# Optimization experiments

Measured on AMD Instinct MI355X. Metric: run time of the kernel, lower is better.

## Reference

```python
import jax, jax.numpy as jnp
import numpy as np

D_MODEL = 1024
N_HEADS = 16
D_K = D_MODEL // N_HEADS
ROPE_BASE = 10000.0


def rope_cos_sin(seq_len, d_k, base=ROPE_BASE, dtype=jnp.float32):
    inv_freq = 1.0 / (base ** (jnp.arange(0, d_k, 2, dtype=dtype) / d_k))  # [d_k/2]
    pos = jnp.arange(seq_len, dtype=dtype)
    freqs = jnp.outer(pos, inv_freq)  # [T, d_k/2]
    return jnp.cos(freqs), jnp.sin(freqs)


def apply_rope(x, cos, sin):
    # x: [B, H, T, d_k]; cos/sin: [T, d_k/2]
    x1 = x[..., 0::2]
    x2 = x[..., 1::2]
    c = cos[None, None]
    s = sin[None, None]
    r1 = x1 * c - x2 * s
    r2 = x1 * s + x2 * c
    # interleave back: stack on new last axis then flatten
    return jnp.stack([r1, r2], axis=-1).reshape(x.shape)


def setup_inputs() -> dict:
    key = jax.random.key(0)
    ks = jax.random.split(key, 7)
    B, T = 2, 2048
    q = jax.random.normal(ks[0], (B, T, D_MODEL), dtype=jnp.float32)
    k = jax.random.normal(ks[1], (B, T, D_MODEL), dtype=jnp.float32)
    v = jax.random.normal(ks[2], (B, T, D_MODEL), dtype=jnp.float32)
    scale = 1.0 / np.sqrt(D_MODEL)
    W_q = jax.random.normal(ks[3], (D_MODEL, D_MODEL), dtype=jnp.float32) * scale
    W_k = jax.random.normal(ks[4], (D_MODEL, D_MODEL), dtype=jnp.float32) * scale
    W_v = jax.random.normal(ks[5], (D_MODEL, D_MODEL), dtype=jnp.float32) * scale
    W_o = jax.random.normal(ks[6], (D_MODEL, D_MODEL), dtype=jnp.float32) * scale
    return {"q": q, "k": k, "v": v, "W_q": W_q, "W_k": W_k, "W_v": W_v, "W_o": W_o}


def reference(q, k, v, W_q, W_k, W_v, W_o):
    B, T_q, _ = q.shape
    T_k = k.shape[1]
    # Linear (torch stores weight as [out, in]; y = x @ W.T)
    Q = (q @ W_q.T).reshape(B, T_q, N_HEADS, D_K).transpose(0, 2, 1, 3)
    K = (k @ W_k.T).reshape(B, T_k, N_HEADS, D_K).transpose(0, 2, 1, 3)
    V = (v @ W_v.T).reshape(B, T_k, N_HEADS, D_K).transpose(0, 2, 1, 3)
    cos_q, sin_q = rope_cos_sin(T_q, D_K)
    cos_k, sin_k = rope_cos_sin(T_k, D_K)
    Q = apply_rope(Q, cos_q, sin_q)
    K = apply_rope(K, cos_k, sin_k)
    scale = jnp.sqrt(jnp.asarray(D_K, dtype=Q.dtype))
    scores = jnp.einsum('bhqd,bhkd->bhqk', Q, K) / scale  # [B,H,Tq,Tk]
    attn = jax.nn.softmax(scores, axis=-1)
    out = jnp.einsum('bhqk,bhkd->bhqd', attn, V)
    out = out.transpose(0, 2, 1, 3).reshape(B, T_q, D_MODEL)
    return out @ W_o.T
```

## Files before the change

kernel.cpp:

```cpp
#include <hip/hip_runtime.h>
#include <math.h>

#define D_MODEL 1024
#define NHEADS  16
#define DK      64
#define TT      2048
#define BB      2
#define MM      (BB * TT)
#define SEG     ((size_t)4194304)
#define WSEG    ((size_t)1048576)

typedef __attribute__((ext_vector_type(8))) short bf16x8;
typedef __attribute__((ext_vector_type(4))) float f32x4;
typedef __attribute__((ext_vector_type(4))) uint  u32x4;

__device__ __forceinline__ ushort f2bf(float f) {
    union { float f; uint u; } v; v.f = f;
    return (ushort)((v.u + 0x7FFFu + ((v.u >> 16) & 1u)) >> 16);
}
__device__ __forceinline__ float bf2f(ushort h) {
    union { uint u; float f; } v; v.u = (uint)h << 16;
    return v.f;
}
__device__ __forceinline__ uint packbf(float lo, float hi) {
    return (uint)f2bf(lo) | ((uint)f2bf(hi) << 16);
}
__device__ __forceinline__ void gld16(ushort* lds, const ushort* g) {
    __builtin_amdgcn_global_load_lds(
        (const __attribute__((address_space(1))) void*)g,
        (__attribute__((address_space(3))) void*)lds, 16, 0, 0);
}
__device__ __forceinline__ void split2(float x, ushort& h, ushort& l) {
    h = f2bf(x);
    l = f2bf(x - bf2f(h));
}

__global__ __launch_bounds__(256) void cast_w_kernel(
    const float* __restrict__ wq, const float* __restrict__ wk,
    const float* __restrict__ wv, const float* __restrict__ wo,
    ushort* __restrict__ WH, ushort* __restrict__ WL)
{
    const int a = blockIdx.y;
    const float* src = (a == 0) ? wq : (a == 1) ? wk : (a == 2) ? wv : wo;
    ushort* hi = WH + (size_t)a * WSEG;
    ushort* lo = WL + (size_t)a * WSEG;
    const size_t i = ((size_t)blockIdx.x * 256 + threadIdx.x) * 8;
#pragma unroll
    for (int c = 0; c < 2; ++c) {
        float4 f = *(const float4*)&src[i + 4 * c];
        ushort4 uh, ul;
        split2(f.x, uh.x, ul.x); split2(f.y, uh.y, ul.y);
        split2(f.z, uh.z, ul.z); split2(f.w, uh.w, ul.w);
        *(ushort4*)&hi[i + 4 * c] = uh;
        *(ushort4*)&lo[i + 4 * c] = ul;
    }
}

__global__ __launch_bounds__(256) void cast_a_kernel(
    const float* __restrict__ src, ushort* __restrict__ hi, ushort* __restrict__ lo)
{
    const size_t i = ((size_t)blockIdx.x * 256 + threadIdx.x) * 8;
#pragma unroll
    for (int c = 0; c < 2; ++c) {
        float4 f = *(const float4*)&src[i + 4 * c];
        ushort4 uh, ul;
        split2(f.x, uh.x, ul.x); split2(f.y, uh.y, ul.y);
        split2(f.z, uh.z, ul.z); split2(f.w, uh.w, ul.w);
        *(ushort4*)&hi[i + 4 * c] = uh;
        *(ushort4*)&lo[i + 4 * c] = ul;
    }
}

template<int MODE>
__global__ __launch_bounds__(256) void gemm_kernel(
    const ushort* __restrict__ Ah, const ushort* __restrict__ Al,
    const ushort* __restrict__ Wh, const ushort* __restrict__ Wl,
    ushort* __restrict__ dst_bf, float* __restrict__ dst_f32)
{
    __shared__ ushort AsH[128 * 64];
    __shared__ ushort AsL[128 * 64];
    __shared__ ushort BsH[128 * 64];
    __shared__ ushort BsL[128 * 64];

    const int tid = threadIdx.x, lane = tid & 63, w = tid >> 6;
    const int g = lane >> 4, l15 = lane & 15;
    const int m0 = blockIdx.y << 7, n0 = blockIdx.x << 7;
    const int mw = (w >> 1) << 6, nw = (w & 1) << 6;

    int sOff[4], sBase[4];
#pragma unroll
    for (int i = 0; i < 4; ++i) {
        const int s = w * 256 + i * 64 + lane;
        const int r = s >> 3;
        sOff[i]  = r * 1024 + (((s & 7) ^ (r & 7)) << 3);
        sBase[i] = (w * 256 + i * 64) << 3;
    }

    const int p0 = (g ^ (l15 & 7)) << 3;
    const int p1 = ((4 + g) ^ (l15 & 7)) << 3;

    f32x4 acc[4][4] = {};

    for (int k0 = 0; k0 < 1024; k0 += 64) {
        const ushort* pA = (size_t)m0 * 1024 + k0 + Ah;
        const ushort* pa = (size_t)m0 * 1024 + k0 + Al;
        const ushort* pW = (size_t)n0 * 1024 + k0 + Wh;
        const ushort* pw = (size_t)n0 * 1024 + k0 + Wl;
#pragma unroll
        for (int i = 0; i < 4; ++i) {
            gld16(&AsH[sBase[i]], pA + sOff[i]);
            gld16(&AsL[sBase[i]], pa + sOff[i]);
            gld16(&BsH[sBase[i]], pW + sOff[i]);
            gld16(&BsL[sBase[i]], pw + sOff[i]);
        }
        __syncthreads();

#pragma unroll
        for (int ks = 0; ks < 2; ++ks) {
            const int pk = ks ? p1 : p0;
            bf16x8 ah[4], al[4];
#pragma unroll
            for (int j = 0; j < 4; ++j) {
                ah[j] = *(const bf16x8*)&AsH[(mw + 16 * j + l15) * 64 + pk];
                al[j] = *(const bf16x8*)&AsL[(mw + 16 * j + l15) * 64 + pk];
            }
#pragma unroll
            for (int i = 0; i < 4; ++i) {
                bf16x8 wh = *(const bf16x8*)&BsH[(nw + 16 * i + l15) * 64 + pk];
                bf16x8 wl = *(const bf16x8*)&BsL[(nw + 16 * i + l15) * 64 + pk];
#pragma unroll
                for (int j = 0; j < 4; ++j) {
                    if (MODE == 1) {
                        acc[j][i] = __builtin_amdgcn_mfma_f32_16x16x32_bf16(ah[j], wh, acc[j][i], 0, 0, 0);
                        acc[j][i] = __builtin_amdgcn_mfma_f32_16x16x32_bf16(ah[j], wl, acc[j][i], 0, 0, 0);
                        acc[j][i] = __builtin_amdgcn_mfma_f32_16x16x32_bf16(al[j], wh, acc[j][i], 0, 0, 0);
                    } else {
                        acc[i][j] = __builtin_amdgcn_mfma_f32_16x16x32_bf16(wh, ah[j], acc[i][j], 0, 0, 0);
                        acc[i][j] = __builtin_amdgcn_mfma_f32_16x16x32_bf16(wl, ah[j], acc[i][j], 0, 0, 0);
                        acc[i][j] = __builtin_amdgcn_mfma_f32_16x16x32_bf16(wh, al[j], acc[i][j], 0, 0, 0);
                    }
                }
            }
        }
        __syncthreads();
    }

    if (MODE == 0) {
        const float lb_over_dk = 9.210340371976184f / 64.0f;
#pragma unroll
        for (int ni = 0; ni < 4; ++ni) {
            const int nG = n0 + nw + 16 * ni + 4 * g;
            const int h  = nG >> 6;
            const int d0 = nG & 63;
            const float inv0 = __expf(-(float)(d0)     * lb_over_dk);
            const float inv1 = __expf(-(float)(d0 + 2) * lb_over_dk);
#pragma unroll
            for (int mj = 0; mj < 4; ++mj) {
                const int tG = m0 + mw + 16 * mj + l15;
                const int t  = tG & (TT - 1);
                const int b  = tG >> 11;
                const f32x4 x = acc[ni][mj];
                float c0, s0, c1, s1;
                __sincosf((float)t * inv0, &s0, &c0);
                __sincosf((float)t * inv1, &s1, &c1);
                ushort4 o;
                o.x = f2bf(x[0] * c0 - x[1] * s0);
                o.y = f2bf(x[0] * s0 + x[1] * c0);
                o.z = f2bf(x[2] * c1 - x[3] * s1);
                o.w = f2bf(x[2] * s1 + x[3] * c1);
                *(ushort4*)&dst_bf[(((size_t)b * NHEADS + h) * TT + t) * DK + d0] = o;
            }
        }
    } else if (MODE == 1) {
#pragma unroll
        for (int mi = 0; mi < 4; ++mi) {
            const int tG = m0 + mw + 16 * mi + 4 * g;
            const int t  = tG & (TT - 1);
            const int b  = tG >> 11;
#pragma unroll
            for (int nj = 0; nj < 4; ++nj) {
                const int nG = n0 + nw + 16 * nj + l15;
                const int h  = nG >> 6;
                const int d  = nG & 63;
                const f32x4 x = acc[mi][nj];
                ushort4 o = {f2bf(x[0]), f2bf(x[1]), f2bf(x[2]), f2bf(x[3])};
                *(ushort4*)&dst_bf[(((size_t)b * NHEADS + h) * DK + d) * TT + t] = o;
            }
        }
    } else {
#pragma unroll
        for (int ni = 0; ni < 4; ++ni) {
            const int nG = n0 + nw + 16 * ni + 4 * g;
#pragma unroll
            for (int mj = 0; mj < 4; ++mj) {
                const int m = m0 + mw + 16 * mj + l15;
                const f32x4 x = acc[ni][mj];
                *(float4*)&dst_f32[(size_t)m * D_MODEL + nG] = make_float4(x[0], x[1], x[2], x[3]);
            }
        }
    }
}

__global__ __launch_bounds__(256) void attn_kernel(
    const ushort* __restrict__ Qw, const ushort* __restrict__ Kw,
    const ushort* __restrict__ Vtw, ushort* __restrict__ ctxH, ushort* __restrict__ ctxL)
{
    __shared__ ushort Ks[64 * 64];
    __shared__ ushort Vs[64 * 64];

    const int tid  = threadIdx.x;
    const int lane = tid & 63;
    const int w    = tid >> 6;
    const int qi   = lane & 15;
    const int g    = lane >> 4;
    const int bh   = blockIdx.y;
    const int q0   = blockIdx.x << 6;

    const ushort* Qp = Qw  + (size_t)bh * TT * DK;
    const ushort* Kp = Kw  + (size_t)bh * TT * DK;
    const ushort* Vp = Vtw + (size_t)bh * DK * TT;

    const int qrow = q0 + w * 16 + qi;
    bf16x8 qf0 = *(const bf16x8*)&Qp[(size_t)qrow * DK + 8 * g];
    bf16x8 qf1 = *(const bf16x8*)&Qp[(size_t)qrow * DK + 32 + 8 * g];

    float m_i = -INFINITY, l_i = 0.0f;
    f32x4 o[4] = {};

    const int c0row = tid >> 3, c0col = tid & 7;
    const int c1row = (tid + 256) >> 3, c1col = tid & 7;
    const int sw0 = (c0col ^ (c0row & 7)) << 3;
    const int sw1 = (c1col ^ (c1row & 7)) << 3;

    for (int kt = 0; kt < TT; kt += 64) {
        *(float4*)&Ks[c0row * 64 + sw0] = *(const float4*)&Kp[(size_t)(kt + c0row) * DK + c0col * 8];
        *(float4*)&Ks[c1row * 64 + sw1] = *(const float4*)&Kp[(size_t)(kt + c1row) * DK + c1col * 8];
        *(float4*)&Vs[c0row * 64 + sw0] = *(const float4*)&Vp[(size_t)c0row * TT + kt + c0col * 8];
        *(float4*)&Vs[c1row * 64 + sw1] = *(const float4*)&Vp[(size_t)c1row * TT + kt + c1col * 8];
        __syncthreads();

        float sv[4][4];
#pragma unroll
        for (int c = 0; c < 4; ++c) {
            f32x4 acc = {};
            const int row = c * 16 + qi;
#pragma unroll
            for (int s = 0; s < 2; ++s) {
                const int col16 = (4 * s + g) ^ (row & 7);
                bf16x8 kf = *(const bf16x8*)&Ks[row * 64 + col16 * 8];
                acc = __builtin_amdgcn_mfma_f32_16x16x32_bf16(kf, (s == 0) ? qf0 : qf1, acc, 0, 0, 0);
            }
#pragma unroll
            for (int r = 0; r < 4; ++r) sv[c][r] = acc[r] * 0.125f;
        }

        float mt = fmaxf(fmaxf(fmaxf(sv[0][0], sv[0][1]), fmaxf(sv[0][2], sv[0][3])),
                         fmaxf(fmaxf(sv[1][0], sv[1][1]), fmaxf(sv[1][2], sv[1][3])));
        mt = fmaxf(mt, fmaxf(fmaxf(fmaxf(sv[2][0], sv[2][1]), fmaxf(sv[2][2], sv[2][3])),
                             fmaxf(fmaxf(sv[3][0], sv[3][1]), fmaxf(sv[3][2], sv[3][3]))));
        mt = fmaxf(mt, __shfl_xor(mt, 16));
        mt = fmaxf(mt, __shfl_xor(mt, 32));
        const float mnew  = fmaxf(m_i, mt);
        const float alpha = __expf(m_i - mnew);
        m_i = mnew;

        float rs = 0.0f;
        uint pp[4][2];
#pragma unroll
        for (int c = 0; c < 4; ++c) {
            float p0 = __expf(sv[c][0] - mnew);
            float p1 = __expf(sv[c][1] - mnew);
            float p2 = __expf(sv[c][2] - mnew);
            float p3 = __expf(sv[c][3] - mnew);
            rs += (p0 + p1) + (p2 + p3);
            pp[c][0] = packbf(p0, p1);
            pp[c][1] = packbf(p2, p3);
        }
        rs += __shfl_xor(rs, 16);
        rs += __shfl_xor(rs, 32);
        l_i = l_i * alpha + rs;
#pragma unroll
        for (int dt = 0; dt < 4; ++dt)
#pragma unroll
            for (int r = 0; r < 4; ++r) o[dt][r] *= alpha;

#pragma unroll
        for (int s = 0; s < 2; ++s) {
            uint bu[4];
#pragma unroll
            for (int v = 0; v < 4; ++v) {
                const int srcl = ((2 * (g & 1) + (v >> 1)) << 4) + qi;
                const uint a = __shfl(pp[2 * s][v & 1], srcl);
                const uint b = __shfl(pp[2 * s + 1][v & 1], srcl);
                bu[v] = (g >> 1) ? b : a;
            }
            u32x4 bu4 = {bu[0], bu[1], bu[2], bu[3]};
            bf16x8 pf = __builtin_bit_cast(bf16x8, bu4);
#pragma unroll
            for (int dt = 0; dt < 4; ++dt) {
                const int row = dt * 16 + qi;
                const int col16 = (4 * s + g) ^ (row & 7);
                bf16x8 vf = *(const bf16x8*)&Vs[row * 64 + col16 * 8];
                o[dt] = __builtin_amdgcn_mfma_f32_16x16x32_bf16(vf, pf, o[dt], 0, 0, 0);
            }
        }
        __syncthreads();
    }

    const float inv = 1.0f / l_i;
    const int b = bh >> 4, h = bh & 15;
    const size_t base = ((size_t)b * TT + qrow) * D_MODEL + h * DK;
#pragma unroll
    for (int dt = 0; dt < 4; ++dt) {
        ushort4 oh, ol;
#pragma unroll
        for (int r = 0; r < 4; ++r) {
            float val = o[dt][r] * inv;
            ushort hh, ll; split2(val, hh, ll);
            ((ushort*)&oh)[r] = hh;
            ((ushort*)&ol)[r] = ll;
        }
        *(ushort4*)&ctxH[base + dt * 16 + 4 * g] = oh;
        *(ushort4*)&ctxL[base + dt * 16 + 4 * g] = ol;
    }
}

extern "C" void kernel_launch(void* const* d_in, const int* in_sizes, int n_in,
                              void* d_out, int out_size, void* d_ws, size_t ws_size,
                              hipStream_t stream)
{
    const float* q   = (const float*)d_in[0];
    const float* k   = (const float*)d_in[1];
    const float* v   = (const float*)d_in[2];
    const float* W_q = (const float*)d_in[3];
    const float* W_k = (const float*)d_in[4];
    const float* W_v = (const float*)d_in[5];
    const float* W_o = (const float*)d_in[6];

    ushort* ws   = (ushort*)d_ws;
    ushort* actH = ws;
    ushort* actL = actH + SEG;
    ushort* WH   = actL + SEG;
    ushort* WL   = WH + 4 * WSEG;
    ushort* Qb   = WL + 4 * WSEG;
    ushort* Kb   = Qb + SEG;
    ushort* Vtb  = Kb + SEG;
    ushort* ctxH = actH;
    ushort* ctxL = actL;

    cast_w_kernel<<<dim3(512, 4), 256, 0, stream>>>(W_q, W_k, W_v, W_o, WH, WL);

    cast_a_kernel<<<2048, 256, 0, stream>>>(q, actH, actL);
    gemm_kernel<0><<<dim3(8, 32), 256, 0, stream>>>(actH, actL, WH, WL, Qb, nullptr);
    cast_a_kernel<<<2048, 256, 0, stream>>>(k, actH, actL);
    gemm_kernel<0><<<dim3(8, 32), 256, 0, stream>>>(actH, actL, WH + WSEG, WL + WSEG, Kb, nullptr);
    cast_a_kernel<<<2048, 256, 0, stream>>>(v, actH, actL);
    gemm_kernel<1><<<dim3(8, 32), 256, 0, stream>>>(actH, actL, WH + 2 * WSEG, WL + 2 * WSEG, Vtb, nullptr);

    attn_kernel<<<dim3(TT / 64, BB * NHEADS), 256, 0, stream>>>(Qb, Kb, Vtb, ctxH, ctxL);

    gemm_kernel<2><<<dim3(8, 32), 256, 0, stream>>>(ctxH, ctxL, WH + 3 * WSEG, WL + 3 * WSEG,
                                                    nullptr, (float*)d_out);
}
```

Before: 355.3 us.

## Double-buffer GEMM shared tiles and batch Q/K projections into one launch

The GEMM main loop now uses two shared-memory buffers, so async global-to-LDS loads for the next k-tile overlap with MFMA work on the current one, and one barrier per stage replaces two. Q and K projections run as a single launch with blockIdx.z selecting the input, weight and output segment, which doubles the grid to 512 blocks and removes one launch. Shared memory grows to 128KB per block, which limits occupancy to one block per CU, and the workspace layout changes so the casted q and k coexist.

```diff
diff --git a/kernel.cpp b/kernel.cpp
--- a/kernel.cpp
+++ b/kernel.cpp
@@ -77,10 +77,17 @@
     const ushort* __restrict__ Wh, const ushort* __restrict__ Wl,
     ushort* __restrict__ dst_bf, float* __restrict__ dst_f32)
 {
-    __shared__ ushort AsH[128 * 64];
-    __shared__ ushort AsL[128 * 64];
-    __shared__ ushort BsH[128 * 64];
-    __shared__ ushort BsL[128 * 64];
+    if (MODE == 0) {
+        const int z = blockIdx.z;
+        Ah += (size_t)z * SEG;  Al += (size_t)z * SEG;
+        Wh += (size_t)z * WSEG; Wl += (size_t)z * WSEG;
+        dst_bf += (size_t)z * SEG;
+    }
+
+    __shared__ ushort AsH0[128 * 64]; __shared__ ushort AsH1[128 * 64];
+    __shared__ ushort AsL0[128 * 64]; __shared__ ushort AsL1[128 * 64];
+    __shared__ ushort BsH0[128 * 64]; __shared__ ushort BsH1[128 * 64];
+    __shared__ ushort BsL0[128 * 64]; __shared__ ushort BsL1[128 * 64];
 
     const int tid = threadIdx.x, lane = tid & 63, w = tid >> 6;
     const int g = lane >> 4, l15 = lane & 15;
@@ -101,33 +108,35 @@
 
     f32x4 acc[4][4] = {};
 
-    for (int k0 = 0; k0 < 1024; k0 += 64) {
-        const ushort* pA = (size_t)m0 * 1024 + k0 + Ah;
-        const ushort* pa = (size_t)m0 * 1024 + k0 + Al;
-        const ushort* pW = (size_t)n0 * 1024 + k0 + Wh;
-        const ushort* pw = (size_t)n0 * 1024 + k0 + Wl;
+    auto stage = [&](ushort* dAH, ushort* dAL, ushort* dBH, ushort* dBL, int k0) {
+        const ushort* pA = Ah + (size_t)m0 * 1024 + k0;
+        const ushort* pa = Al + (size_t)m0 * 1024 + k0;
+        const ushort* pW = Wh + (size_t)n0 * 1024 + k0;
+        const ushort* pw = Wl + (size_t)n0 * 1024 + k0;
 #pragma unroll
         for (int i = 0; i < 4; ++i) {
-            gld16(&AsH[sBase[i]], pA + sOff[i]);
-            gld16(&AsL[sBase[i]], pa + sOff[i]);
-            gld16(&BsH[sBase[i]], pW + sOff[i]);
-            gld16(&BsL[sBase[i]], pw + sOff[i]);
-        }
-        __syncthreads();
-
+            gld16(dAH + sBase[i], pA + sOff[i]);
+            gld16(dAL + sBase[i], pa + sOff[i]);
+            gld16(dBH + sBase[i], pW + sOff[i]);
+            gld16(dBL + sBase[i], pw + sOff[i]);
+        }
+    };
+
+    auto compute = [&](const ushort* aH, const ushort* aL,
+                       const ushort* bH, const ushort* bL) {
 #pragma unroll
         for (int ks = 0; ks < 2; ++ks) {
             const int pk = ks ? p1 : p0;
             bf16x8 ah[4], al[4];
 #pragma unroll
             for (int j = 0; j < 4; ++j) {
-                ah[j] = *(const bf16x8*)&AsH[(mw + 16 * j + l15) * 64 + pk];
-                al[j] = *(const bf16x8*)&AsL[(mw + 16 * j + l15) * 64 + pk];
+                ah[j] = *(const bf16x8*)&aH[(mw + 16 * j + l15) * 64 + pk];
+                al[j] = *(const bf16x8*)&aL[(mw + 16 * j + l15) * 64 + pk];
             }
 #pragma unroll
             for (int i = 0; i < 4; ++i) {
-                bf16x8 wh = *(const bf16x8*)&BsH[(nw + 16 * i + l15) * 64 + pk];
-                bf16x8 wl = *(const bf16x8*)&BsL[(nw + 16 * i + l15) * 64 + pk];
+                bf16x8 wh = *(const bf16x8*)&bH[(nw + 16 * i + l15) * 64 + pk];
+                bf16x8 wl = *(const bf16x8*)&bL[(nw + 16 * i + l15) * 64 + pk];
 #pragma unroll
                 for (int j = 0; j < 4; ++j) {
                     if (MODE == 1) {
@@ -142,6 +151,19 @@
                 }
             }
         }
+    };
+
+    stage(AsH0, AsL0, BsH0, BsL0, 0);
+    __syncthreads();
+
+#pragma unroll
+    for (int it = 0; it < 8; ++it) {
+        const int k0 = it * 128;
+        stage(AsH1, AsL1, BsH1, BsL1, k0 + 64);
+        compute(AsH0, AsL0, BsH0, BsL0);
+        __syncthreads();
+        if (it < 7) stage(AsH0, AsL0, BsH0, BsL0, k0 + 128);
+        compute(AsH1, AsL1, BsH1, BsL1);
         __syncthreads();
     }
 
@@ -337,25 +359,25 @@
     const float* W_v = (const float*)d_in[5];
     const float* W_o = (const float*)d_in[6];
 
-    ushort* ws   = (ushort*)d_ws;
-    ushort* actH = ws;
-    ushort* actL = actH + SEG;
-    ushort* WH   = actL + SEG;
-    ushort* WL   = WH + 4 * WSEG;
-    ushort* Qb   = WL + 4 * WSEG;
-    ushort* Kb   = Qb + SEG;
-    ushort* Vtb  = Kb + SEG;
-    ushort* ctxH = actH;
-    ushort* ctxL = actL;
+    ushort* ws  = (ushort*)d_ws;
+    ushort* AH  = ws;
+    ushort* AL  = AH + 2 * SEG;
+    ushort* WH  = AL + 2 * SEG;
+    ushort* WL  = WH + 4 * WSEG;
+    ushort* Qb  = WL + 4 * WSEG;
+    ushort* Kb  = Qb + SEG;
+    ushort* Vtb = Kb + SEG;
+    ushort* ctxH = AH + SEG;
+    ushort* ctxL = AL + SEG;
 
     cast_w_kernel<<<dim3(512, 4), 256, 0, stream>>>(W_q, W_k, W_v, W_o, WH, WL);
 
-    cast_a_kernel<<<2048, 256, 0, stream>>>(q, actH, actL);
-    gemm_kernel<0><<<dim3(8, 32), 256, 0, stream>>>(actH, actL, WH, WL, Qb, nullptr);
-    cast_a_kernel<<<2048, 256, 0, stream>>>(k, actH, actL);
-    gemm_kernel<0><<<dim3(8, 32), 256, 0, stream>>>(actH, actL, WH + WSEG, WL + WSEG, Kb, nullptr);
-    cast_a_kernel<<<2048, 256, 0, stream>>>(v, actH, actL);
-    gemm_kernel<1><<<dim3(8, 32), 256, 0, stream>>>(actH, actL, WH + 2 * WSEG, WL + 2 * WSEG, Vtb, nullptr);
+    cast_a_kernel<<<2048, 256, 0, stream>>>(q, AH, AL);
+    cast_a_kernel<<<2048, 256, 0, stream>>>(k, AH + SEG, AL + SEG);
+    gemm_kernel<0><<<dim3(8, 32, 2), 256, 0, stream>>>(AH, AL, WH, WL, Qb, nullptr);
+
+    cast_a_kernel<<<2048, 256, 0, stream>>>(v, AH, AL);
+    gemm_kernel<1><<<dim3(8, 32), 256, 0, stream>>>(AH, AL, WH + 2 * WSEG, WL + 2 * WSEG, Vtb, nullptr);
 
     attn_kernel<<<dim3(TT / 64, BB * NHEADS), 256, 0, stream>>>(Qb, Kb, Vtb, ctxH, ctxL);
 
```

New measurement: 337.0 us. 5.1% less time.
